# Performance work log

Measured on AMD Instinct MI355X. Metric: run time of the kernel, lower is better.

## Reference

```python
import jax, jax.numpy as jnp
import numpy as np

N = 50000   # n_nodes (== input_dim, featureless identity features)
E = 800000  # edges per support (avg degree 16)
D = 200     # embed_dim (hardcoded in GIN)
C = 10      # num_classes


def setup_inputs() -> dict:
    key = jax.random.key(0)
    ks = jax.random.split(key, 8)
    x = jnp.zeros((N, 1), jnp.float32)  # unused: layer 0 is featureless
    rows0 = jax.random.randint(ks[0], (E,), 0, N, dtype=jnp.int32)
    cols0 = jax.random.randint(ks[1], (E,), 0, N, dtype=jnp.int32)
    vals0 = jax.random.uniform(ks[2], (E,), jnp.float32)
    rows1 = jax.random.randint(ks[3], (E,), 0, N, dtype=jnp.int32)
    cols1 = jax.random.randint(ks[4], (E,), 0, N, dtype=jnp.int32)
    vals1 = jax.random.uniform(ks[5], (E,), jnp.float32)
    W0 = jax.random.normal(ks[6], (N, D), jnp.float32) * 0.02
    W1 = jax.random.normal(ks[7], (D, C), jnp.float32) * 0.05
    eps0 = jnp.zeros((1,), jnp.float32)  # train_eps init (~1e-4 in repo)
    eps1 = jnp.zeros((1,), jnp.float32)
    return dict(x=x, rows0=rows0, cols0=cols0, vals0=vals0,
                rows1=rows1, cols1=cols1, vals1=vals1,
                W0=W0, W1=W1, eps0=eps0, eps1=eps1)


def reference(x, rows0, cols0, vals0, rows1, cols1, vals1, W0, W1, eps0, eps1):
    # sparse A @ X via gather + segment-sum (A in COO: rows, cols, vals)
    def spmm(r, c, v, X):
        return jax.ops.segment_sum(v[:, None] * X[c], r, num_segments=N)

    # Layer 0 (featureless, num_mlp_layers==1):
    #   AX = sum_i A_i ; out = AX @ W0 + 0.1*(1+eps0)*W0
    h0 = spmm(rows0, cols0, vals0, W0) + spmm(rows1, cols1, vals1, W0) \
         + 0.1 * (1.0 + eps0[0]) * W0
    h = jax.nn.relu(h0)  # [N, D]

    # Layer 1 (with features): out = (sum_i A_i @ h + 0.1*(1+eps1)*h) @ W1
    ax = spmm(rows0, cols0, vals0, h) + spmm(rows1, cols1, vals1, h)
    out = (ax + 0.1 * (1.0 + eps1[0]) * h) @ W1  # [N, C]
    return out
```

## Files before the change

kernel.cpp:

```cpp
#include <hip/hip_runtime.h>

#define N_NODES 50000
#define E_EDGES 800000
#define E2      (2 * E_EDGES)
#define D_DIM   200
#define C_CLS   10
#define NB_BUCKET 196
#define BATCH     4096
#define NB_SCATTER ((E2 + BATCH - 1) / BATCH)
#define NB_CONV    ((N_NODES * D_DIM / 4 + 255) / 256)
#define CAP       12288
#define NWIN      13

static __device__ __forceinline__ unsigned f2bf(float f) {
    unsigned u = __float_as_uint(f);
    return (u + 0x7FFFu + ((u >> 16) & 1u)) >> 16;
}
static __device__ __forceinline__ float bf_lo(unsigned u) {
    return __uint_as_float(u << 16);
}
static __device__ __forceinline__ float bf_hi(unsigned u) {
    return __uint_as_float(u & 0xFFFF0000u);
}

__global__ __launch_bounds__(256) void convert_scatter_kernel(
        const float* __restrict__ W0, unsigned short* __restrict__ W0h,
        const int* __restrict__ rows0, const int* __restrict__ cols0,
        const float* __restrict__ vals0,
        const int* __restrict__ rows1, const int* __restrict__ cols1,
        const float* __restrict__ vals1,
        int* __restrict__ bcur,
        int2* __restrict__ stage) {
    __shared__ int cntL[NB_BUCKET];
    __shared__ int baseL[NB_BUCKET];
    __shared__ int offL[NB_BUCKET];
    __shared__ int2 recL[BATCH];

    if (blockIdx.x >= NB_SCATTER) {
        int i = ((blockIdx.x - NB_SCATTER) * 256 + threadIdx.x) * 4;
        if (i < N_NODES * D_DIM) {
            float4 f = *(const float4*)(W0 + i);
            uint2 p;
            p.x = f2bf(f.x) | (f2bf(f.y) << 16);
            p.y = f2bf(f.z) | (f2bf(f.w) << 16);
            *(uint2*)(W0h + i) = p;
        }
        return;
    }

    const int tid = threadIdx.x;
    const int e0 = blockIdx.x * BATCH;

    for (int b = tid; b < NB_BUCKET; b += 256) cntL[b] = 0;
    __syncthreads();

#pragma unroll
    for (int k = 0; k < BATCH / 256; ++k) {
        int idx = k * 256 + tid;
        int e = e0 + idx;
        if (e < E2) {
            int r, c;
            float v;
            if (e < E_EDGES) {
                r = rows0[e]; c = cols0[e]; v = vals0[e];
            } else {
                int e1 = e - E_EDGES;
                r = rows1[e1]; c = cols1[e1]; v = vals1[e1];
            }
            recL[idx] = make_int2((int)((unsigned)r | ((unsigned)c << 16)),
                                  __float_as_int(v));
            atomicAdd(&cntL[r >> 8], 1);
        }
    }
    __syncthreads();

    for (int b = tid; b < NB_BUCKET; b += 256) {
        int c = cntL[b];
        baseL[b] = (c > 0) ? atomicAdd(&bcur[b], c) : 0;
        offL[b] = 0;
    }
    __syncthreads();

#pragma unroll
    for (int k = 0; k < BATCH / 256; ++k) {
        int idx = k * 256 + tid;
        int e = e0 + idx;
        if (e < E2) {
            int2 rec = recL[idx];
            int b = (int)(((unsigned)rec.x & 0xFFFFu) >> 8);
            int pos = baseL[b] + atomicAdd(&offL[b], 1);
            stage[(size_t)b * CAP + pos] = rec;
        }
    }
}

__global__ __launch_bounds__(256) void build_csr_kernel(
        const int* __restrict__ bcur,
        const int2* __restrict__ stage,
        int* __restrict__ ticket,
        int2* __restrict__ rowseg,
        unsigned* __restrict__ cv4) {
    __shared__ int hist[256 * NWIN];
    __shared__ int ws4[4];
    __shared__ int sbase;
    const int b = blockIdx.x;
    const int tid = threadIdx.x;
    const int lane = tid & 63;
    const int w = tid >> 6;

    for (int i = tid; i < 256 * NWIN; i += 256) hist[i] = 0;
    __syncthreads();

    const int n = bcur[b];
    const int2* __restrict__ sp = stage + (size_t)b * CAP;
    for (int i = tid; i < n; i += 256) {
        unsigned u = (unsigned)sp[i].x;
        atomicAdd(&hist[(u & 255u) * NWIN + (u >> 28)], 1);
    }
    __syncthreads();

    int rowtot = 0;
#pragma unroll
    for (int k = 0; k < NWIN; ++k) rowtot += hist[tid * NWIN + k];

    int v = rowtot;
#pragma unroll
    for (int off = 1; off < 64; off <<= 1) {
        int t = __shfl_up(v, off, 64);
        if (lane >= off) v += t;
    }
    if (lane == 63) ws4[w] = v;
    __syncthreads();
    if (tid == 0) {
        int s = 0;
#pragma unroll
        for (int k = 0; k < 4; ++k) { int t = ws4[k]; ws4[k] = s; s += t; }
    }
    __syncthreads();
    v += ws4[w];

    if (tid == 255) sbase = atomicAdd(ticket, v);
    __syncthreads();

    const int start = sbase + v - rowtot;
    const int row = (b << 8) + tid;
    if (row < N_NODES) rowseg[row] = make_int2(start, rowtot);

    int c = start;
#pragma unroll
    for (int k = 0; k < NWIN; ++k) {
        int t = hist[tid * NWIN + k];
        hist[tid * NWIN + k] = c;
        c += t;
    }
    __syncthreads();

    for (int i = tid; i < n; i += 256) {
        int2 rec = sp[i];
        unsigned u = (unsigned)rec.x;
        int pos = atomicAdd(&hist[(u & 255u) * NWIN + (u >> 28)], 1);
        cv4[pos] = (u & 0xFFFF0000u) | f2bf(__int_as_float(rec.y));
    }
}

__global__ __launch_bounds__(256) void spmm_layer0_fused_kernel(
        const int2* __restrict__ rowseg,
        const unsigned* __restrict__ cv4,
        const unsigned short* __restrict__ W0h,
        const float* __restrict__ W1,
        const float* __restrict__ eps0,
        float* __restrict__ g) {
    __shared__ __align__(16) float W1Ts[C_CLS * D_DIM];
    for (int i = threadIdx.x; i < C_CLS * D_DIM; i += 256) {
        int k = i / D_DIM, d = i - k * D_DIM;
        W1Ts[i] = W1[d * C_CLS + k];
    }
    __syncthreads();

    const int lane = threadIdx.x & 63;
    const int n = __builtin_amdgcn_readfirstlane(blockIdx.x * 4 + (threadIdx.x >> 6));
    if (n >= N_NODES) return;
    const float s0 = 0.1f * (1.0f + eps0[0]);
    const bool act = (lane < 50);
    const uint2* __restrict__ F = (const uint2*)W0h;

    const int2 seg = rowseg[n];
    const int beg  = seg.x;
    const int endp = seg.x + seg.y;
    float a0 = 0.f, a1 = 0.f, a2 = 0.f, a3 = 0.f;

    int e = beg;
    for (; e + 8 <= endp; e += 8) {
        unsigned w0 = cv4[e],     w1 = cv4[e + 1], w2 = cv4[e + 2], w3 = cv4[e + 3];
        unsigned w4 = cv4[e + 4], w5 = cv4[e + 5], w6 = cv4[e + 6], w7 = cv4[e + 7];
        if (act) {
            uint2 u0 = F[(size_t)(w0 >> 16) * 50 + lane];
            uint2 u1 = F[(size_t)(w1 >> 16) * 50 + lane];
            uint2 u2 = F[(size_t)(w2 >> 16) * 50 + lane];
            uint2 u3 = F[(size_t)(w3 >> 16) * 50 + lane];
            uint2 u4 = F[(size_t)(w4 >> 16) * 50 + lane];
            uint2 u5 = F[(size_t)(w5 >> 16) * 50 + lane];
            uint2 u6 = F[(size_t)(w6 >> 16) * 50 + lane];
            uint2 u7 = F[(size_t)(w7 >> 16) * 50 + lane];
            float v0 = __uint_as_float(w0 << 16), v1 = __uint_as_float(w1 << 16);
            float v2 = __uint_as_float(w2 << 16), v3 = __uint_as_float(w3 << 16);
            float v4 = __uint_as_float(w4 << 16), v5 = __uint_as_float(w5 << 16);
            float v6 = __uint_as_float(w6 << 16), v7 = __uint_as_float(w7 << 16);
            a0 += v0 * bf_lo(u0.x) + v1 * bf_lo(u1.x) + v2 * bf_lo(u2.x) + v3 * bf_lo(u3.x)
                + v4 * bf_lo(u4.x) + v5 * bf_lo(u5.x) + v6 * bf_lo(u6.x) + v7 * bf_lo(u7.x);
            a1 += v0 * bf_hi(u0.x) + v1 * bf_hi(u1.x) + v2 * bf_hi(u2.x) + v3 * bf_hi(u3.x)
                + v4 * bf_hi(u4.x) + v5 * bf_hi(u5.x) + v6 * bf_hi(u6.x) + v7 * bf_hi(u7.x);
            a2 += v0 * bf_lo(u0.y) + v1 * bf_lo(u1.y) + v2 * bf_lo(u2.y) + v3 * bf_lo(u3.y)
                + v4 * bf_lo(u4.y) + v5 * bf_lo(u5.y) + v6 * bf_lo(u6.y) + v7 * bf_lo(u7.y);
            a3 += v0 * bf_hi(u0.y) + v1 * bf_hi(u1.y) + v2 * bf_hi(u2.y) + v3 * bf_hi(u3.y)
                + v4 * bf_hi(u4.y) + v5 * bf_hi(u5.y) + v6 * bf_hi(u6.y) + v7 * bf_hi(u7.y);
        }
    }
    for (; e + 4 <= endp; e += 4) {
        unsigned w0 = cv4[e], w1 = cv4[e + 1], w2 = cv4[e + 2], w3 = cv4[e + 3];
        if (act) {
            uint2 u0 = F[(size_t)(w0 >> 16) * 50 + lane];
            uint2 u1 = F[(size_t)(w1 >> 16) * 50 + lane];
            uint2 u2 = F[(size_t)(w2 >> 16) * 50 + lane];
            uint2 u3 = F[(size_t)(w3 >> 16) * 50 + lane];
            float v0 = __uint_as_float(w0 << 16), v1 = __uint_as_float(w1 << 16);
            float v2 = __uint_as_float(w2 << 16), v3 = __uint_as_float(w3 << 16);
            a0 += v0 * bf_lo(u0.x) + v1 * bf_lo(u1.x) + v2 * bf_lo(u2.x) + v3 * bf_lo(u3.x);
            a1 += v0 * bf_hi(u0.x) + v1 * bf_hi(u1.x) + v2 * bf_hi(u2.x) + v3 * bf_hi(u3.x);
            a2 += v0 * bf_lo(u0.y) + v1 * bf_lo(u1.y) + v2 * bf_lo(u2.y) + v3 * bf_lo(u3.y);
            a3 += v0 * bf_hi(u0.y) + v1 * bf_hi(u1.y) + v2 * bf_hi(u2.y) + v3 * bf_hi(u3.y);
        }
    }
    for (; e < endp; ++e) {
        unsigned w = cv4[e];
        if (act) {
            uint2 u = F[(size_t)(w >> 16) * 50 + lane];
            float v = __uint_as_float(w << 16);
            a0 += v * bf_lo(u.x);
            a1 += v * bf_hi(u.x);
            a2 += v * bf_lo(u.y);
            a3 += v * bf_hi(u.y);
        }
    }

    float o[C_CLS];
#pragma unroll
    for (int k = 0; k < C_CLS; ++k) o[k] = 0.f;

    const float4* __restrict__ W1T4 = (const float4*)W1Ts;
    if (act) {
        uint2 w = F[(size_t)n * 50 + lane];
        a0 = fmaxf(a0 + s0 * bf_lo(w.x), 0.f);
        a1 = fmaxf(a1 + s0 * bf_hi(w.x), 0.f);
        a2 = fmaxf(a2 + s0 * bf_lo(w.y), 0.f);
        a3 = fmaxf(a3 + s0 * bf_hi(w.y), 0.f);
#pragma unroll
        for (int k = 0; k < C_CLS; ++k) {
            float4 wv = W1T4[k * 50 + lane];
            o[k] = a0 * wv.x + a1 * wv.y + a2 * wv.z + a3 * wv.w;
        }
    }

#pragma unroll
    for (int k = 0; k < C_CLS; ++k) {
        for (int off = 32; off > 0; off >>= 1)
            o[k] += __shfl_xor(o[k], off, 64);
    }

    if (lane == 0) {
        float* gp = g + (size_t)n * C_CLS;
#pragma unroll
        for (int k = 0; k < C_CLS; ++k) gp[k] = o[k];
    }
}

__global__ __launch_bounds__(256) void spmm_layer1_light_kernel(
        const int2* __restrict__ rowseg,
        const unsigned* __restrict__ cv4,
        const float* __restrict__ g,
        const float* __restrict__ eps1,
        float* __restrict__ out) {
    const int lane = threadIdx.x & 63;
    const int n = __builtin_amdgcn_readfirstlane(blockIdx.x * 4 + (threadIdx.x >> 6));
    if (n >= N_NODES) return;
    const int grp = lane / 10;
    const int d   = lane - grp * 10;
    const float s1 = 0.1f * (1.0f + eps1[0]);

    const int2 seg = rowseg[n];
    const int beg  = seg.x;
    const int endp = seg.x + seg.y;
    float acc = 0.f;

    for (int base = beg; base < endp; base += 12) {
        if (grp < 6) {
            int ea = base + grp;
            int eb = base + 6 + grp;
            unsigned pa = (ea < endp) ? cv4[ea] : 0u;
            unsigned pb = (eb < endp) ? cv4[eb] : 0u;
            if (ea < endp)
                acc += __uint_as_float(pa << 16) * g[(size_t)(pa >> 16) * C_CLS + d];
            if (eb < endp)
                acc += __uint_as_float(pb << 16) * g[(size_t)(pb >> 16) * C_CLS + d];
        }
    }

    float t;
    t = __shfl(acc, lane + 10, 64); if (lane < 50) acc += t;
    t = __shfl(acc, lane + 20, 64); if (lane < 30) acc += t;
    t = __shfl(acc, lane + 40, 64); if (lane < 10) acc += t;

    if (lane < 10) {
        out[(size_t)n * C_CLS + d] = acc + s1 * g[(size_t)n * C_CLS + d];
    }
}

extern "C" void kernel_launch(void* const* d_in, const int* in_sizes, int n_in,
                              void* d_out, int out_size, void* d_ws, size_t ws_size,
                              hipStream_t stream) {
    const int*   rows0 = (const int*)d_in[1];
    const int*   cols0 = (const int*)d_in[2];
    const float* vals0 = (const float*)d_in[3];
    const int*   rows1 = (const int*)d_in[4];
    const int*   cols1 = (const int*)d_in[5];
    const float* vals1 = (const float*)d_in[6];
    const float* W0    = (const float*)d_in[7];
    const float* W1    = (const float*)d_in[8];
    const float* eps0  = (const float*)d_in[9];
    const float* eps1  = (const float*)d_in[10];
    float* out = (float*)d_out;

    char* ws = (char*)d_ws;
    size_t off = 0;
    auto alloc = [&](size_t bytes) {
        void* p = ws + off;
        off += (bytes + 255) & ~(size_t)255;
        return p;
    };
    unsigned short* W0h = (unsigned short*)alloc((size_t)N_NODES * D_DIM * 2);
    float* g      = (float*)alloc((size_t)N_NODES * C_CLS * 4);
    int2* rowseg  = (int2*)alloc((size_t)N_NODES * 8);
    int* bcur     = (int*)alloc((size_t)(NB_BUCKET + 1) * 4);
    unsigned* cv4 = (unsigned*)alloc((size_t)E2 * 4);
    int2* stage   = (int2*)alloc((size_t)NB_BUCKET * CAP * 8);
    int* ticket   = bcur + NB_BUCKET;
    (void)ws_size;

    hipMemsetAsync(bcur, 0, (size_t)(NB_BUCKET + 1) * 4, stream);
    convert_scatter_kernel<<<NB_SCATTER + NB_CONV, 256, 0, stream>>>(
        W0, W0h, rows0, cols0, vals0, rows1, cols1, vals1, bcur, stage);
    build_csr_kernel<<<NB_BUCKET, 256, 0, stream>>>(bcur, stage, ticket, rowseg, cv4);

    const int spmm_grid = (N_NODES + 3) / 4;
    spmm_layer0_fused_kernel<<<spmm_grid, 256, 0, stream>>>(
        rowseg, cv4, W0h, W1, eps0, g);
    spmm_layer1_light_kernel<<<spmm_grid, 256, 0, stream>>>(
        rowseg, cv4, g, eps1, out);
}
```

Baseline: 272.0 us.

## Replace bucketed two-pass CSR build with global row histogram, scan, and atomic placement

Replaces the bucket scatter plus per-bucket LDS counting sort with three kernels: a per-row global atomic histogram fused with the W0 bf16 conversion, a block scan that assigns row starts via a ticket atomic, and a placement kernel that writes each packed edge using a per-row global atomic cursor. This removes the staging buffer and its round trip through memory, but uses about 3.2M global atomics on random addresses instead of LDS atomics. Edge order within a row becomes nondeterministic, and rows are still grouped in 256-row blocks in whatever order the tickets are handed out.

```diff
diff --git a/kernel.cpp b/kernel.cpp
--- a/kernel.cpp
+++ b/kernel.cpp
@@ -5,12 +5,9 @@
 #define E2      (2 * E_EDGES)
 #define D_DIM   200
 #define C_CLS   10
-#define NB_BUCKET 196
-#define BATCH     4096
-#define NB_SCATTER ((E2 + BATCH - 1) / BATCH)
-#define NB_CONV    ((N_NODES * D_DIM / 4 + 255) / 256)
-#define CAP       12288
-#define NWIN      13
+#define NB_EDGE 782
+#define NB_CONV ((N_NODES * D_DIM / 4 + 255) / 256)
+#define NB_SCAN ((N_NODES + 255) / 256)
 
 static __device__ __forceinline__ unsigned f2bf(float f) {
     unsigned u = __float_as_uint(f);
@@ -23,21 +20,12 @@
     return __uint_as_float(u & 0xFFFF0000u);
 }
 
-__global__ __launch_bounds__(256) void convert_scatter_kernel(
+__global__ __launch_bounds__(256) void hist_convert_kernel(
         const float* __restrict__ W0, unsigned short* __restrict__ W0h,
-        const int* __restrict__ rows0, const int* __restrict__ cols0,
-        const float* __restrict__ vals0,
-        const int* __restrict__ rows1, const int* __restrict__ cols1,
-        const float* __restrict__ vals1,
-        int* __restrict__ bcur,
-        int2* __restrict__ stage) {
-    __shared__ int cntL[NB_BUCKET];
-    __shared__ int baseL[NB_BUCKET];
-    __shared__ int offL[NB_BUCKET];
-    __shared__ int2 recL[BATCH];
-
-    if (blockIdx.x >= NB_SCATTER) {
-        int i = ((blockIdx.x - NB_SCATTER) * 256 + threadIdx.x) * 4;
+        const int* __restrict__ rows0, const int* __restrict__ rows1,
+        int* __restrict__ rowcnt) {
+    if (blockIdx.x >= NB_EDGE) {
+        int i = ((blockIdx.x - NB_EDGE) * 256 + threadIdx.x) * 4;
         if (i < N_NODES * D_DIM) {
             float4 f = *(const float4*)(W0 + i);
             uint2 p;
@@ -47,17 +35,67 @@
         }
         return;
     }
-
+    const int base = blockIdx.x * 2048;
+#pragma unroll
+    for (int k = 0; k < 8; ++k) {
+        int e = base + k * 256 + threadIdx.x;
+        if (e < E2) {
+            int r = (e < E_EDGES) ? rows0[e] : rows1[e - E_EDGES];
+            atomicAdd(&rowcnt[r], 1);
+        }
+    }
+}
+
+__global__ __launch_bounds__(256) void scan_kernel(
+        const int* __restrict__ rowcnt,
+        int* __restrict__ ticket,
+        int2* __restrict__ rowseg,
+        int* __restrict__ rowcur) {
+    __shared__ int ws4[4];
+    __shared__ int sbase;
     const int tid = threadIdx.x;
-    const int e0 = blockIdx.x * BATCH;
-
-    for (int b = tid; b < NB_BUCKET; b += 256) cntL[b] = 0;
+    const int lane = tid & 63;
+    const int w = tid >> 6;
+    const int row = blockIdx.x * 256 + tid;
+    const int cnt = (row < N_NODES) ? rowcnt[row] : 0;
+
+    int v = cnt;
+#pragma unroll
+    for (int off = 1; off < 64; off <<= 1) {
+        int t = __shfl_up(v, off, 64);
+        if (lane >= off) v += t;
+    }
+    if (lane == 63) ws4[w] = v;
     __syncthreads();
-
-#pragma unroll
-    for (int k = 0; k < BATCH / 256; ++k) {
-        int idx = k * 256 + tid;
-        int e = e0 + idx;
+    if (tid == 0) {
+        int s = 0;
+#pragma unroll
+        for (int k = 0; k < 4; ++k) { int t = ws4[k]; ws4[k] = s; s += t; }
+    }
+    __syncthreads();
+    v += ws4[w];
+
+    if (tid == 255) sbase = atomicAdd(ticket, v);
+    __syncthreads();
+
+    const int start = sbase + v - cnt;
+    if (row < N_NODES) {
+        rowseg[row] = make_int2(start, cnt);
+        rowcur[row] = start;
+    }
+}
+
+__global__ __launch_bounds__(256) void place_kernel(
+        const int* __restrict__ rows0, const int* __restrict__ cols0,
+        const float* __restrict__ vals0,
+        const int* __restrict__ rows1, const int* __restrict__ cols1,
+        const float* __restrict__ vals1,
+        int* __restrict__ rowcur,
+        unsigned* __restrict__ cv4) {
+    const int base = blockIdx.x * 2048;
+#pragma unroll
+    for (int k = 0; k < 8; ++k) {
+        int e = base + k * 256 + threadIdx.x;
         if (e < E2) {
             int r, c;
             float v;
@@ -67,99 +105,9 @@
                 int e1 = e - E_EDGES;
                 r = rows1[e1]; c = cols1[e1]; v = vals1[e1];
             }
-            recL[idx] = make_int2((int)((unsigned)r | ((unsigned)c << 16)),
-                                  __float_as_int(v));
-            atomicAdd(&cntL[r >> 8], 1);
-        }
-    }
-    __syncthreads();
-
-    for (int b = tid; b < NB_BUCKET; b += 256) {
-        int c = cntL[b];
-        baseL[b] = (c > 0) ? atomicAdd(&bcur[b], c) : 0;
-        offL[b] = 0;
-    }
-    __syncthreads();
-
-#pragma unroll
-    for (int k = 0; k < BATCH / 256; ++k) {
-        int idx = k * 256 + tid;
-        int e = e0 + idx;
-        if (e < E2) {
-            int2 rec = recL[idx];
-            int b = (int)(((unsigned)rec.x & 0xFFFFu) >> 8);
-            int pos = baseL[b] + atomicAdd(&offL[b], 1);
-            stage[(size_t)b * CAP + pos] = rec;
-        }
-    }
-}
-
-__global__ __launch_bounds__(256) void build_csr_kernel(
-        const int* __restrict__ bcur,
-        const int2* __restrict__ stage,
-        int* __restrict__ ticket,
-        int2* __restrict__ rowseg,
-        unsigned* __restrict__ cv4) {
-    __shared__ int hist[256 * NWIN];
-    __shared__ int ws4[4];
-    __shared__ int sbase;
-    const int b = blockIdx.x;
-    const int tid = threadIdx.x;
-    const int lane = tid & 63;
-    const int w = tid >> 6;
-
-    for (int i = tid; i < 256 * NWIN; i += 256) hist[i] = 0;
-    __syncthreads();
-
-    const int n = bcur[b];
-    const int2* __restrict__ sp = stage + (size_t)b * CAP;
-    for (int i = tid; i < n; i += 256) {
-        unsigned u = (unsigned)sp[i].x;
-        atomicAdd(&hist[(u & 255u) * NWIN + (u >> 28)], 1);
-    }
-    __syncthreads();
-
-    int rowtot = 0;
-#pragma unroll
-    for (int k = 0; k < NWIN; ++k) rowtot += hist[tid * NWIN + k];
-
-    int v = rowtot;
-#pragma unroll
-    for (int off = 1; off < 64; off <<= 1) {
-        int t = __shfl_up(v, off, 64);
-        if (lane >= off) v += t;
-    }
-    if (lane == 63) ws4[w] = v;
-    __syncthreads();
-    if (tid == 0) {
-        int s = 0;
-#pragma unroll
-        for (int k = 0; k < 4; ++k) { int t = ws4[k]; ws4[k] = s; s += t; }
-    }
-    __syncthreads();
-    v += ws4[w];
-
-    if (tid == 255) sbase = atomicAdd(ticket, v);
-    __syncthreads();
-
-    const int start = sbase + v - rowtot;
-    const int row = (b << 8) + tid;
-    if (row < N_NODES) rowseg[row] = make_int2(start, rowtot);
-
-    int c = start;
-#pragma unroll
-    for (int k = 0; k < NWIN; ++k) {
-        int t = hist[tid * NWIN + k];
-        hist[tid * NWIN + k] = c;
-        c += t;
-    }
-    __syncthreads();
-
-    for (int i = tid; i < n; i += 256) {
-        int2 rec = sp[i];
-        unsigned u = (unsigned)rec.x;
-        int pos = atomicAdd(&hist[(u & 255u) * NWIN + (u >> 28)], 1);
-        cv4[pos] = (u & 0xFFFF0000u) | f2bf(__int_as_float(rec.y));
+            int pos = atomicAdd(&rowcur[r], 1);
+            cv4[pos] = ((unsigned)c << 16) | f2bf(v);
+        }
     }
 }
 
@@ -340,16 +288,18 @@
     unsigned short* W0h = (unsigned short*)alloc((size_t)N_NODES * D_DIM * 2);
     float* g      = (float*)alloc((size_t)N_NODES * C_CLS * 4);
     int2* rowseg  = (int2*)alloc((size_t)N_NODES * 8);
-    int* bcur     = (int*)alloc((size_t)(NB_BUCKET + 1) * 4);
+    int* rowcnt   = (int*)alloc((size_t)(N_NODES + 1) * 4);
+    int* rowcur   = (int*)alloc((size_t)N_NODES * 4);
     unsigned* cv4 = (unsigned*)alloc((size_t)E2 * 4);
-    int2* stage   = (int2*)alloc((size_t)NB_BUCKET * CAP * 8);
-    int* ticket   = bcur + NB_BUCKET;
+    int* ticket   = rowcnt + N_NODES;
     (void)ws_size;
 
-    hipMemsetAsync(bcur, 0, (size_t)(NB_BUCKET + 1) * 4, stream);
-    convert_scatter_kernel<<<NB_SCATTER + NB_CONV, 256, 0, stream>>>(
-        W0, W0h, rows0, cols0, vals0, rows1, cols1, vals1, bcur, stage);
-    build_csr_kernel<<<NB_BUCKET, 256, 0, stream>>>(bcur, stage, ticket, rowseg, cv4);
+    hipMemsetAsync(rowcnt, 0, (size_t)(N_NODES + 1) * 4, stream);
+    hist_convert_kernel<<<NB_EDGE + NB_CONV, 256, 0, stream>>>(
+        W0, W0h, rows0, rows1, rowcnt);
+    scan_kernel<<<NB_SCAN, 256, 0, stream>>>(rowcnt, ticket, rowseg, rowcur);
+    place_kernel<<<NB_EDGE, 256, 0, stream>>>(
+        rows0, cols0, vals0, rows1, cols1, vals1, rowcur, cv4);
 
     const int spmm_grid = (N_NODES + 3) / 4;
     spmm_layer0_fused_kernel<<<spmm_grid, 256, 0, stream>>>(
```

Result: slower. 415.4 us (+52.7%).
